# Optimization experiments

Measured on AMD Instinct MI355X. Metric: run time of the kernel, lower is better.

Reference implementation:

```python
import jax, jax.numpy as jnp
import numpy as np

B, L, V, D = 8, 128, 32000, 64
R1, R2, UP = 2 * D, 5 * D, 10 * D  # first_reduce, second_reduce, up_scale defaults


def pos_enc(seq_len, d, n=10000.0):
    # matches getPositionEncoding: P[k,2i]=sin(k/n^(2i/d)), P[k,2i+1]=cos(k/n^(2i/d))
    k = jnp.arange(seq_len, dtype=jnp.float32)[:, None]
    i = jnp.arange(d // 2, dtype=jnp.float32)[None, :]
    ang = k / (n ** (2.0 * i / d))
    return jnp.stack([jnp.sin(ang), jnp.cos(ang)], axis=-1).reshape(seq_len, d)


def setup_inputs() -> dict:
    key = jax.random.key(0)
    ks = jax.random.split(key, 20)

    def lin(k, out_f, in_f):
        bound = 1.0 / np.sqrt(in_f)
        k1, k2 = jax.random.split(k)
        W = jax.random.uniform(k1, (out_f, in_f), jnp.float32, -bound, bound)
        b = jax.random.uniform(k2, (out_f,), jnp.float32, -bound, bound)
        return W, b

    inp = {"x": jax.random.uniform(ks[0], (B, L, V), jnp.float32)}
    inp["W_emb"], inp["b_emb"] = lin(ks[1], D, V)
    inp["W_pos1"], inp["b_pos1"] = lin(ks[2], D, 2 * D)
    inp["W_red"], inp["b_red"] = lin(ks[3], R1, L * D)
    inp["W_pos2"], inp["b_pos2"] = lin(ks[4], R1, 2 * R1)
    inp["W_red2"], inp["b_red2"] = lin(ks[5], R2, L * R1)
    inp["W_pos3"], inp["b_pos3"] = lin(ks[6], R2, 2 * R2)
    inp["W_up1"], inp["b_up1"] = lin(ks[7], UP, R2)
    inp["W_up2"], inp["b_up2"] = lin(ks[8], V, UP)
    inp["W_fin"], inp["b_fin"] = lin(ks[9], 1, L)
    return inp


def reference(x, W_emb, b_emb, W_pos1, b_pos1, W_red, b_red, W_pos2, b_pos2,
              W_red2, b_red2, W_pos3, b_pos3, W_up1, b_up1, W_up2, b_up2,
              W_fin, b_fin):
    relu = jax.nn.relu
    P1 = pos_enc(L, 2 * D)   # [L, 2D]
    P2 = pos_enc(L, 2 * R1)  # [L, 2*R1]
    P3 = pos_enc(L, 2 * R2)  # [L, 2*R2]

    h = relu(x @ W_emb.T + b_emb)                       # [B, L, D]
    h = h + relu(P1 @ W_pos1.T + b_pos1)[None]          # learned sin pos emb

    # einsum('bij,bkm->bikj'): out[b,i,k,j] = h[b,i,j] * sum_m h[b,k,m]
    s = h.sum(-1)                                       # [B, L]
    h = (h[:, :, None, :] * s[:, None, :, None]).reshape(B, L, L * D)
    h = relu(h @ W_red.T + b_red)                       # [B, L, R1]
    h = h + relu(P2 @ W_pos2.T + b_pos2)[None]

    s = h.sum(-1)                                       # [B, L]
    h = (h[:, :, None, :] * s[:, None, :, None]).reshape(B, L, L * R1)
    h = relu(h @ W_red2.T + b_red2)                     # [B, L, R2]
    h = h + relu(P3 @ W_pos3.T + b_pos3)[None]

    h = relu(h @ W_up1.T + b_up1)                       # [B, L, UP]
    h = relu(h @ W_up2.T + b_up2)                       # [B, L, V]
    # transpose(1,2) then Linear(L->1), relu, squeeze
    out = relu(jnp.einsum('blv,l->bv', h, W_fin[0]) + b_fin[0])  # [B, V]
    return out
```

## Files before the change

kernel.cpp:

```cpp
#include <hip/hip_runtime.h>
#include <hip/hip_bf16.h>
#include <math.h>

#define B_  8
#define L_  128
#define V_  32000
#define D_  64
#define R1_ 128
#define R2_ 320
#define UP_ 640
#define SPLITS_ 50

typedef short bf16x8 __attribute__((ext_vector_type(8)));
typedef float f32x4 __attribute__((ext_vector_type(4)));

#define GLDS16(gp, lp)                                                         \
    __builtin_amdgcn_global_load_lds(                                          \
        (const __attribute__((address_space(1))) void*)(gp),                   \
        (__attribute__((address_space(3))) void*)(lp), 16, 0, 0)

static __device__ inline unsigned short f2bf(float x) {
    __hip_bfloat16 h = __float2bfloat16(x);
    return *reinterpret_cast<unsigned short*>(&h);
}

static __device__ inline void split1(float v, unsigned short& h, unsigned short& l) {
    unsigned short hb = f2bf(v);
    float hf = __uint_as_float(((unsigned int)hb) << 16);
    h = hb;
    l = f2bf(v - hf);
}

__global__ __launch_bounds__(256) void prep_weights(const float* __restrict__ Wemb,
                                                    unsigned short* __restrict__ Whb,
                                                    unsigned short* __restrict__ Wlb,
                                                    const float* __restrict__ Wup2,
                                                    unsigned short* __restrict__ Wup2b) {
    int bx = blockIdx.x, t = threadIdx.x;
    if (bx < 1000) {
        int u = bx * 256 + t;
        int kb = u >> 6, row = u & 63;
        const float* s = Wemb + (size_t)row * 32000 + kb * 8;
        unsigned short h8[8], l8[8];
#pragma unroll
        for (int j = 0; j < 8; ++j) split1(s[j], h8[j], l8[j]);
        *(ushort4*)&Whb[(size_t)u * 8]     = *(ushort4*)&h8[0];
        *(ushort4*)&Whb[(size_t)u * 8 + 4] = *(ushort4*)&h8[4];
        *(ushort4*)&Wlb[(size_t)u * 8]     = *(ushort4*)&l8[0];
        *(ushort4*)&Wlb[(size_t)u * 8 + 4] = *(ushort4*)&l8[4];
    } else {
        const int n4 = (V_ * UP_) / 4;
        int stride = 4096 * 256;
        for (int i = (bx - 1000) * 256 + t; i < n4; i += stride) {
            float4 v = ((const float4*)Wup2)[i];
            ushort4 o;
            o.x = f2bf(v.x); o.y = f2bf(v.y); o.z = f2bf(v.z); o.w = f2bf(v.w);
            ((ushort4*)Wup2b)[i] = o;
        }
    }
}

__global__ __launch_bounds__(320) void pe_all(const float* __restrict__ W1,
                                              const float* __restrict__ b1,
                                              float* __restrict__ o1,
                                              const float* __restrict__ W2,
                                              const float* __restrict__ b2,
                                              float* __restrict__ o2,
                                              const float* __restrict__ W3,
                                              const float* __restrict__ b3,
                                              float* __restrict__ o3) {
    __shared__ float P[640];
    int l = blockIdx.x;
    int stage = blockIdx.y;
    const float* W = (stage == 0) ? W1 : (stage == 1) ? W2 : W3;
    const float* bias = (stage == 0) ? b1 : (stage == 1) ? b2 : b3;
    float* out = (stage == 0) ? o1 : (stage == 1) ? o2 : o3;
    int outF = (stage == 0) ? 64 : (stage == 1) ? 128 : 320;
    int dEnc = 2 * outF;
    int t = threadIdx.x;
    for (int m = t; m < dEnc; m += 320) {
        int i = m >> 1;
        float ang = (float)l * powf(10000.0f, -2.0f * (float)i / (float)dEnc);
        P[m] = (m & 1) ? cosf(ang) : sinf(ang);
    }
    __syncthreads();
    if (t < outF) {
        float acc = bias[t];
        const float4* w = (const float4*)(W + (size_t)t * dEnc);
        for (int m4 = 0; m4 < dEnc / 4; ++m4) {
            float4 wv = w[m4];
            float4 pv = *(const float4*)&P[m4 * 4];
            acc = fmaf(pv.x, wv.x, acc);
            acc = fmaf(pv.y, wv.y, acc);
            acc = fmaf(pv.z, wv.z, acc);
            acc = fmaf(pv.w, wv.w, acc);
        }
        out[l * outF + t] = fmaxf(acc, 0.f);
    }
}

__global__ __launch_bounds__(256) void embA_mfma(const float* __restrict__ x,
                                                 const unsigned short* __restrict__ Whb,
                                                 const unsigned short* __restrict__ Wlb,
                                                 float* __restrict__ partA) {
    __shared__ short lds[16384];
    int t = threadIdx.x;
    int lane = t & 63, w = t >> 6;
    int ln = lane & 15, lg = lane >> 4;
    int rb = blockIdx.x, ks = blockIdx.y;
    int row0 = rb * 64;
    const float* xrow = x + (size_t)(row0 + w * 16 + ln) * 32000;

    f32x4 acc[4];
#pragma unroll
    for (int nt = 0; nt < 4; ++nt) acc[nt] = (f32x4){0.f, 0.f, 0.f, 0.f};

    float4 xc[4], xn[4];
    {
        int kb0 = (ks * 640) >> 3;
#pragma unroll
        for (int s = 0; s < 4; ++s) {
            int ubase = s * 256 + w * 64;
            const unsigned short* arr = (s < 2) ? Whb : Wlb;
            int uu = (s < 2) ? ubase : (ubase - 512);
            const char* gp = (const char*)arr + ((size_t)kb0 * 64 + uu + lane) * 16;
            char* lp = (char*)lds + ((s < 2) ? 0 : 8192) + uu * 16;
            GLDS16(gp, lp);
        }
        const float* bp = xrow + ks * 640 + lg * 8;
        xc[0] = ((const float4*)bp)[0];
        xc[1] = ((const float4*)bp)[1];
        xc[2] = ((const float4*)(bp + 32))[0];
        xc[3] = ((const float4*)(bp + 32))[1];
    }

#pragma unroll 2
    for (int ch = 0; ch < 10; ++ch) {
        __syncthreads();
        if (ch < 9) {
            int kb0 = (ks * 640 + (ch + 1) * 64) >> 3;
            int p = (ch + 1) & 1;
#pragma unroll
            for (int s = 0; s < 4; ++s) {
                int ubase = s * 256 + w * 64;
                const unsigned short* arr = (s < 2) ? Whb : Wlb;
                int uu = (s < 2) ? ubase : (ubase - 512);
                const char* gp = (const char*)arr + ((size_t)kb0 * 64 + uu + lane) * 16;
                char* lp = (char*)lds + p * 16384 + ((s < 2) ? 0 : 8192) + uu * 16;
                GLDS16(gp, lp);
            }
            const float* bp = xrow + ks * 640 + (ch + 1) * 64 + lg * 8;
            xn[0] = ((const float4*)bp)[0];
            xn[1] = ((const float4*)bp)[1];
            xn[2] = ((const float4*)(bp + 32))[0];
            xn[3] = ((const float4*)(bp + 32))[1];
        }
        bf16x8 ah[2], al[2];
#pragma unroll
        for (int kstep = 0; kstep < 2; ++kstep) {
            float f[8] = {xc[2 * kstep].x, xc[2 * kstep].y, xc[2 * kstep].z, xc[2 * kstep].w,
                          xc[2 * kstep + 1].x, xc[2 * kstep + 1].y, xc[2 * kstep + 1].z,
                          xc[2 * kstep + 1].w};
            unsigned short h8[8], l8[8];
#pragma unroll
            for (int j = 0; j < 8; ++j) split1(f[j], h8[j], l8[j]);
            ah[kstep] = *(bf16x8*)h8;
            al[kstep] = *(bf16x8*)l8;
        }
        const char* buf = (const char*)lds + (ch & 1) * 16384;
#pragma unroll
        for (int kstep = 0; kstep < 2; ++kstep) {
            int g = kstep * 4 + lg;
#pragma unroll
            for (int nt = 0; nt < 4; ++nt) {
                int nrow = nt * 16 + ln;
                bf16x8 bh = *(const bf16x8*)(buf + (g * 64 + nrow) * 16);
                bf16x8 bl = *(const bf16x8*)(buf + 8192 + (g * 64 + nrow) * 16);
                acc[nt] = __builtin_amdgcn_mfma_f32_16x16x32_bf16(ah[kstep], bh, acc[nt], 0, 0, 0);
                acc[nt] = __builtin_amdgcn_mfma_f32_16x16x32_bf16(ah[kstep], bl, acc[nt], 0, 0, 0);
                acc[nt] = __builtin_amdgcn_mfma_f32_16x16x32_bf16(al[kstep], bh, acc[nt], 0, 0, 0);
            }
        }
#pragma unroll
        for (int i = 0; i < 4; ++i) xc[i] = xn[i];
    }
#pragma unroll
    for (int nt = 0; nt < 4; ++nt)
#pragma unroll
        for (int r = 0; r < 4; ++r)
            partA[((size_t)ks * 1024 + row0 + w * 16 + lg * 4 + r) * 64 + nt * 16 + ln] =
                acc[nt][r];
}

__global__ __launch_bounds__(64) void reduceA_kernel(const float* __restrict__ partA,
                                                     const float* __restrict__ bemb,
                                                     const float* __restrict__ pe1,
                                                     float* __restrict__ h1,
                                                     float* __restrict__ s1) {
    int row = blockIdx.x;
    int d = threadIdx.x;
    int l = row & 127;
    float v = bemb[d];
#pragma unroll 5
    for (int s = 0; s < SPLITS_; ++s) v += partA[((size_t)s * 1024 + row) * 64 + d];
    v = fmaxf(v, 0.f) + pe1[l * 64 + d];
    h1[row * 64 + d] = v;
    float sum = v;
    for (int off = 32; off > 0; off >>= 1) sum += __shfl_down(sum, off);
    if (d == 0) s1[row] = sum;
}

__global__ __launch_bounds__(64) void wr1_kernel(const float* __restrict__ Wred,
                                                 const float* __restrict__ s1,
                                                 float* __restrict__ Wr1) {
    __shared__ float ss[8 * 128];
    int r = blockIdx.x;
    int j = threadIdx.x;
    for (int idx = j; idx < 1024; idx += 64) ss[idx] = s1[idx];
    __syncthreads();
    float acc[8];
#pragma unroll
    for (int b = 0; b < 8; ++b) acc[b] = 0.f;
    const float* w = Wred + (size_t)r * 8192 + j;
    for (int k = 0; k < 128; ++k) {
        float wv = w[k * 64];
#pragma unroll
        for (int b = 0; b < 8; ++b) acc[b] = fmaf(ss[b * 128 + k], wv, acc[b]);
    }
#pragma unroll
    for (int b = 0; b < 8; ++b) Wr1[((size_t)b * 128 + r) * 64 + j] = acc[b];
}

__global__ __launch_bounds__(128) void h2_kernel(const float* __restrict__ h1,
                                                 const float* __restrict__ Wr1,
                                                 const float* __restrict__ bred,
                                                 const float* __restrict__ pe2,
                                                 float* __restrict__ h2,
                                                 float* __restrict__ s2) {
    __shared__ float hrow[64];
    __shared__ float red[2];
    int row = blockIdx.x;
    int b = row >> 7, i = row & 127;
    int r = threadIdx.x;
    if (r < 64) hrow[r] = h1[row * 64 + r];
    __syncthreads();
    float acc = bred[r];
    const float4* w = (const float4*)(Wr1 + ((size_t)b * 128 + r) * 64);
#pragma unroll
    for (int j4 = 0; j4 < 16; ++j4) {
        float4 wv = w[j4];
        float4 hv = *(const float4*)&hrow[j4 * 4];
        acc = fmaf(hv.x, wv.x, acc);
        acc = fmaf(hv.y, wv.y, acc);
        acc = fmaf(hv.z, wv.z, acc);
        acc = fmaf(hv.w, wv.w, acc);
    }
    float val = fmaxf(acc, 0.f) + pe2[i * 128 + r];
    h2[row * 128 + r] = val;
    float sum = val;
    for (int off = 32; off > 0; off >>= 1) sum += __shfl_down(sum, off);
    if ((r & 63) == 0) red[r >> 6] = sum;
    __syncthreads();
    if (r == 0) s2[row] = red[0] + red[1];
}

__global__ __launch_bounds__(128) void wr2_kernel(const float* __restrict__ Wred2,
                                                  const float* __restrict__ s2,
                                                  float* __restrict__ Wr2) {
    __shared__ float ss[8 * 128];
    int r = blockIdx.x;
    int j = threadIdx.x;
    for (int idx = j; idx < 1024; idx += 128) ss[idx] = s2[idx];
    __syncthreads();
    float acc[8];
#pragma unroll
    for (int b = 0; b < 8; ++b) acc[b] = 0.f;
    const float* w = Wred2 + (size_t)r * 16384 + j;
    for (int k = 0; k < 128; ++k) {
        float wv = w[k * 128];
#pragma unroll
        for (int b = 0; b < 8; ++b) acc[b] = fmaf(ss[b * 128 + k], wv, acc[b]);
    }
#pragma unroll
    for (int b = 0; b < 8; ++b) Wr2[((size_t)b * 320 + r) * 128 + j] = acc[b];
}

__global__ __launch_bounds__(320) void h3_kernel(const float* __restrict__ h2,
                                                 const float* __restrict__ Wr2,
                                                 const float* __restrict__ bred2,
                                                 const float* __restrict__ pe3,
                                                 float* __restrict__ h3) {
    __shared__ float hrow[128];
    int row = blockIdx.x;
    int b = row >> 7, i = row & 127;
    int r = threadIdx.x;
    if (r < 128) hrow[r] = h2[row * 128 + r];
    __syncthreads();
    float acc = bred2[r];
    const float4* w = (const float4*)(Wr2 + ((size_t)b * 320 + r) * 128);
#pragma unroll
    for (int j4 = 0; j4 < 32; ++j4) {
        float4 wv = w[j4];
        float4 hv = *(const float4*)&hrow[j4 * 4];
        acc = fmaf(hv.x, wv.x, acc);
        acc = fmaf(hv.y, wv.y, acc);
        acc = fmaf(hv.z, wv.z, acc);
        acc = fmaf(hv.w, wv.w, acc);
    }
    h3[(size_t)row * 320 + r] = fmaxf(acc, 0.f) + pe3[i * 320 + r];
}

__global__ __launch_bounds__(320) void h4_kernel(const float* __restrict__ h3,
                                                 const float* __restrict__ Wup1,
                                                 const float* __restrict__ bup1,
                                                 unsigned short* __restrict__ h4b) {
    __shared__ float hsT[320 * 4];
    int t = threadIdx.x;
    int row0 = blockIdx.x * 4;
    int u = blockIdx.y * 320 + t;
    for (int idx = t; idx < 1280; idx += 320) {
        int q = idx / 320, j = idx - q * 320;
        hsT[j * 4 + q] = h3[(size_t)(row0 + q) * 320 + j];
    }
    __syncthreads();
    float acc[4] = {0.f, 0.f, 0.f, 0.f};
    const float4* w = (const float4*)(Wup1 + (size_t)u * 320);
#pragma unroll 2
    for (int j4 = 0; j4 < 80; ++j4) {
        float4 wv = w[j4];
#pragma unroll
        for (int e = 0; e < 4; ++e) {
            float wc = (e == 0) ? wv.x : (e == 1) ? wv.y : (e == 2) ? wv.z : wv.w;
            float4 hv = *(const float4*)&hsT[(j4 * 4 + e) * 4];
            acc[0] = fmaf(hv.x, wc, acc[0]);
            acc[1] = fmaf(hv.y, wc, acc[1]);
            acc[2] = fmaf(hv.z, wc, acc[2]);
            acc[3] = fmaf(hv.w, wc, acc[3]);
        }
    }
    float bias = bup1[u];
#pragma unroll
    for (int q = 0; q < 4; ++q)
        h4b[(size_t)(row0 + q) * 640 + u] = f2bf(fmaxf(acc[q] + bias, 0.f));
}

__global__ __launch_bounds__(512) void final_mfma_kernel(
    const unsigned short* __restrict__ h4b,
    const unsigned short* __restrict__ Wup2b,
    const float* __restrict__ bup2,
    const float* __restrict__ Wfin,
    const float* __restrict__ bfin,
    float* __restrict__ out) {
    __shared__ short tile[24576];
    __shared__ float redbuf[2][2][128];

    int t = threadIdx.x;
    int lane = t & 63;
    int w = t >> 6;
    int wv = w >> 2;
    int wq = w & 3;
    int bl_ = wq >> 1, lh = wq & 1;
    int ln = lane & 15, lg = lane >> 4;
    int b0 = blockIdx.y * 2;
    int v0 = blockIdx.x * 128;

    f32x4 acc[4][4];
#pragma unroll
    for (int mt = 0; mt < 4; ++mt)
#pragma unroll
        for (int nt = 0; nt < 4; ++nt) acc[mt][nt] = (f32x4){0.f, 0.f, 0.f, 0.f};

    for (int ch = 0; ch < 10; ++ch) {
        int k0 = ch * 64;
        __syncthreads();
#pragma unroll
        for (int s = 0; s < 6; ++s) {
            int F = (w * 6 + s) * 1024 + lane * 16;
            int region = F >> 14;
            int rr = (F >> 7) & 127;
            int g = ((F >> 4) & 7) ^ (rr & 7);
            size_t rowG = (region == 0) ? (size_t)(v0 + rr)
                                        : (size_t)((b0 + region - 1) * 128 + rr);
            const unsigned short* base = (region == 0) ? Wup2b : h4b;
            const char* gp = (const char*)base + (rowG * 640 + (size_t)(k0 + g * 8)) * 2;
            char* lp = (char*)tile + (w * 6 + s) * 1024;
            GLDS16(gp, lp);
        }
        __syncthreads();
#pragma unroll
        for (int ks = 0; ks < 2; ++ks) {
            bf16x8 aF[4], bF[4];
#pragma unroll
            for (int mt = 0; mt < 4; ++mt) {
                int rA = wv * 64 + mt * 16 + ln;
                int g = ks * 4 + lg;
                int off = rA * 128 + ((g ^ (rA & 7)) * 16);
                aF[mt] = *(const bf16x8*)((const char*)tile + off);
            }
#pragma unroll
            for (int nt = 0; nt < 4; ++nt) {
                int rB = lh * 64 + nt * 16 + ln;
                int g = ks * 4 + lg;
                int off = (1 + bl_) * 16384 + rB * 128 + ((g ^ (rB & 7)) * 16);
                bF[nt] = *(const bf16x8*)((const char*)tile + off);
            }
#pragma unroll
            for (int mt = 0; mt < 4; ++mt)
#pragma unroll
                for (int nt = 0; nt < 4; ++nt)
                    acc[mt][nt] = __builtin_amdgcn_mfma_f32_16x16x32_bf16(
                        aF[mt], bF[nt], acc[mt][nt], 0, 0, 0);
        }
    }

    float bfin0 = bfin[0];
#pragma unroll
    for (int mt = 0; mt < 4; ++mt) {
        float bu[4];
#pragma unroll
        for (int r = 0; r < 4; ++r)
            bu[r] = bup2[v0 + wv * 64 + mt * 16 + lg * 4 + r];
        float part[4] = {0.f, 0.f, 0.f, 0.f};
#pragma unroll
        for (int nt = 0; nt < 4; ++nt) {
            float wf = Wfin[lh * 64 + nt * 16 + ln];
#pragma unroll
            for (int r = 0; r < 4; ++r)
                part[r] += wf * fmaxf(acc[mt][nt][r] + bu[r], 0.f);
        }
#pragma unroll
        for (int off = 8; off >= 1; off >>= 1)
#pragma unroll
            for (int r = 0; r < 4; ++r) part[r] += __shfl_xor(part[r], off, 64);
        if (ln == 0) {
#pragma unroll
            for (int r = 0; r < 4; ++r)
                redbuf[bl_][lh][wv * 64 + mt * 16 + lg * 4 + r] = part[r];
        }
    }
    __syncthreads();
    if (t < 256) {
        int bb = t >> 7, v = t & 127;
        float vsum = redbuf[bb][0][v] + redbuf[bb][1][v] + bfin0;
        out[(size_t)(b0 + bb) * 32000 + v0 + v] = fmaxf(vsum, 0.f);
    }
}

extern "C" void kernel_launch(void* const* d_in, const int* in_sizes, int n_in,
                              void* d_out, int out_size, void* d_ws, size_t ws_size,
                              hipStream_t stream) {
    const float* x      = (const float*)d_in[0];
    const float* W_emb  = (const float*)d_in[1];
    const float* b_emb  = (const float*)d_in[2];
    const float* W_pos1 = (const float*)d_in[3];
    const float* b_pos1 = (const float*)d_in[4];
    const float* W_red  = (const float*)d_in[5];
    const float* b_red  = (const float*)d_in[6];
    const float* W_pos2 = (const float*)d_in[7];
    const float* b_pos2 = (const float*)d_in[8];
    const float* W_red2 = (const float*)d_in[9];
    const float* b_red2 = (const float*)d_in[10];
    const float* W_pos3 = (const float*)d_in[11];
    const float* b_pos3 = (const float*)d_in[12];
    const float* W_up1  = (const float*)d_in[13];
    const float* b_up1  = (const float*)d_in[14];
    const float* W_up2  = (const float*)d_in[15];
    const float* b_up2  = (const float*)d_in[16];
    const float* W_fin  = (const float*)d_in[17];
    const float* b_fin  = (const float*)d_in[18];
    float* out = (float*)d_out;

    float* ws  = (float*)d_ws;
    float* pe1 = ws;
    float* pe2 = pe1 + 8192;
    float* pe3 = pe2 + 16384;
    float* h1  = pe3 + 40960;
    float* s1  = h1 + 65536;
    float* Wr1 = s1 + 1024;
    float* h2  = Wr1 + 65536;
    float* s2  = h2 + 131072;
    float* Wr2 = s2 + 1024;
    float* h3  = Wr2 + 327680;
    unsigned short* h4b   = (unsigned short*)(h3 + 327680);
    unsigned short* Wup2b = (unsigned short*)((float*)h4b + 327680);
    float* after = (float*)Wup2b + 10240000;
    unsigned short* Whb = (unsigned short*)after;
    unsigned short* Wlb = Whb + 2048000;
    float* partA = (float*)(Wlb + 2048000);

    prep_weights<<<dim3(5096), 256, 0, stream>>>(W_emb, Whb, Wlb, W_up2, Wup2b);
    pe_all<<<dim3(128, 3), 320, 0, stream>>>(W_pos1, b_pos1, pe1, W_pos2, b_pos2,
                                             pe2, W_pos3, b_pos3, pe3);
    embA_mfma<<<dim3(16, SPLITS_), 256, 0, stream>>>(x, Whb, Wlb, partA);
    reduceA_kernel<<<dim3(1024), 64, 0, stream>>>(partA, b_emb, pe1, h1, s1);
    wr1_kernel<<<dim3(128), 64, 0, stream>>>(W_red, s1, Wr1);
    h2_kernel<<<dim3(1024), 128, 0, stream>>>(h1, Wr1, b_red, pe2, h2, s2);
    wr2_kernel<<<dim3(320), 128, 0, stream>>>(W_red2, s2, Wr2);
    h3_kernel<<<dim3(1024), 320, 0, stream>>>(h2, Wr2, b_red2, pe3, h3);
    h4_kernel<<<dim3(256, 2), 320, 0, stream>>>(h3, W_up1, b_up1, h4b);
    final_mfma_kernel<<<dim3(250, 4), 512, 0, stream>>>(h4b, Wup2b, b_up2, W_fin,
                                                        b_fin, out);
}
```

Measured before the change: 472.9 us.

## Double-buffer final MFMA K-loop, merge prep and pos-enc kernels, add unrolls

The final GEMM's LDS tile is split into two half-size buffers with 32-wide K chunks, so the global-to-LDS load of the next chunk is issued before computing on the current one, and one barrier per iteration is dropped. The weight-prep and positional-encoding kernels are merged into a single launch with 320-thread blocks, removing one kernel launch. Unroll pragmas are added or raised in the reduce and Wr kernels. Smaller K chunks double the iteration count and barriers, and the merged prep kernel makes every block allocate shared memory and use the larger block size.

```diff
diff --git a/kernel.cpp b/kernel.cpp
--- a/kernel.cpp
+++ b/kernel.cpp
@@ -31,14 +31,24 @@
     l = f2bf(v - hf);
 }
 
-__global__ __launch_bounds__(256) void prep_weights(const float* __restrict__ Wemb,
-                                                    unsigned short* __restrict__ Whb,
-                                                    unsigned short* __restrict__ Wlb,
-                                                    const float* __restrict__ Wup2,
-                                                    unsigned short* __restrict__ Wup2b) {
+__global__ __launch_bounds__(320) void prep_all(const float* __restrict__ Wemb,
+                                                unsigned short* __restrict__ Whb,
+                                                unsigned short* __restrict__ Wlb,
+                                                const float* __restrict__ Wup2,
+                                                unsigned short* __restrict__ Wup2b,
+                                                const float* __restrict__ W1,
+                                                const float* __restrict__ b1,
+                                                float* __restrict__ o1,
+                                                const float* __restrict__ W2,
+                                                const float* __restrict__ b2,
+                                                float* __restrict__ o2,
+                                                const float* __restrict__ W3,
+                                                const float* __restrict__ b3,
+                                                float* __restrict__ o3) {
+    __shared__ float P[640];
     int bx = blockIdx.x, t = threadIdx.x;
-    if (bx < 1000) {
-        int u = bx * 256 + t;
+    if (bx < 800) {
+        int u = bx * 320 + t;
         int kb = u >> 6, row = u & 63;
         const float* s = Wemb + (size_t)row * 32000 + kb * 8;
         unsigned short h8[8], l8[8];
@@ -48,54 +58,43 @@
         *(ushort4*)&Whb[(size_t)u * 8 + 4] = *(ushort4*)&h8[4];
         *(ushort4*)&Wlb[(size_t)u * 8]     = *(ushort4*)&l8[0];
         *(ushort4*)&Wlb[(size_t)u * 8 + 4] = *(ushort4*)&l8[4];
+    } else if (bx < 1184) {
+        int id = bx - 800;
+        int l = id & 127;
+        int stage = id >> 7;
+        const float* W = (stage == 0) ? W1 : (stage == 1) ? W2 : W3;
+        const float* bias = (stage == 0) ? b1 : (stage == 1) ? b2 : b3;
+        float* out = (stage == 0) ? o1 : (stage == 1) ? o2 : o3;
+        int outF = (stage == 0) ? 64 : (stage == 1) ? 128 : 320;
+        int dEnc = 2 * outF;
+        for (int m = t; m < dEnc; m += 320) {
+            int i = m >> 1;
+            float ang = (float)l * powf(10000.0f, -2.0f * (float)i / (float)dEnc);
+            P[m] = (m & 1) ? cosf(ang) : sinf(ang);
+        }
+        __syncthreads();
+        if (t < outF) {
+            float acc = bias[t];
+            const float4* w = (const float4*)(W + (size_t)t * dEnc);
+            for (int m4 = 0; m4 < dEnc / 4; ++m4) {
+                float4 wv = w[m4];
+                float4 pv = *(const float4*)&P[m4 * 4];
+                acc = fmaf(pv.x, wv.x, acc);
+                acc = fmaf(pv.y, wv.y, acc);
+                acc = fmaf(pv.z, wv.z, acc);
+                acc = fmaf(pv.w, wv.w, acc);
+            }
+            out[l * outF + t] = fmaxf(acc, 0.f);
+        }
     } else {
         const int n4 = (V_ * UP_) / 4;
-        int stride = 4096 * 256;
-        for (int i = (bx - 1000) * 256 + t; i < n4; i += stride) {
+        int stride = 3200 * 320;
+        for (int i = (bx - 1184) * 320 + t; i < n4; i += stride) {
             float4 v = ((const float4*)Wup2)[i];
             ushort4 o;
             o.x = f2bf(v.x); o.y = f2bf(v.y); o.z = f2bf(v.z); o.w = f2bf(v.w);
             ((ushort4*)Wup2b)[i] = o;
         }
-    }
-}
-
-__global__ __launch_bounds__(320) void pe_all(const float* __restrict__ W1,
-                                              const float* __restrict__ b1,
-                                              float* __restrict__ o1,
-                                              const float* __restrict__ W2,
-                                              const float* __restrict__ b2,
-                                              float* __restrict__ o2,
-                                              const float* __restrict__ W3,
-                                              const float* __restrict__ b3,
-                                              float* __restrict__ o3) {
-    __shared__ float P[640];
-    int l = blockIdx.x;
-    int stage = blockIdx.y;
-    const float* W = (stage == 0) ? W1 : (stage == 1) ? W2 : W3;
-    const float* bias = (stage == 0) ? b1 : (stage == 1) ? b2 : b3;
-    float* out = (stage == 0) ? o1 : (stage == 1) ? o2 : o3;
-    int outF = (stage == 0) ? 64 : (stage == 1) ? 128 : 320;
-    int dEnc = 2 * outF;
-    int t = threadIdx.x;
-    for (int m = t; m < dEnc; m += 320) {
-        int i = m >> 1;
-        float ang = (float)l * powf(10000.0f, -2.0f * (float)i / (float)dEnc);
-        P[m] = (m & 1) ? cosf(ang) : sinf(ang);
-    }
-    __syncthreads();
-    if (t < outF) {
-        float acc = bias[t];
-        const float4* w = (const float4*)(W + (size_t)t * dEnc);
-        for (int m4 = 0; m4 < dEnc / 4; ++m4) {
-            float4 wv = w[m4];
-            float4 pv = *(const float4*)&P[m4 * 4];
-            acc = fmaf(pv.x, wv.x, acc);
-            acc = fmaf(pv.y, wv.y, acc);
-            acc = fmaf(pv.z, wv.z, acc);
-            acc = fmaf(pv.w, wv.w, acc);
-        }
-        out[l * outF + t] = fmaxf(acc, 0.f);
     }
 }
 
@@ -201,7 +200,7 @@
     int d = threadIdx.x;
     int l = row & 127;
     float v = bemb[d];
-#pragma unroll 5
+#pragma unroll 10
     for (int s = 0; s < SPLITS_; ++s) v += partA[((size_t)s * 1024 + row) * 64 + d];
     v = fmaxf(v, 0.f) + pe1[l * 64 + d];
     h1[row * 64 + d] = v;
@@ -222,6 +221,7 @@
 #pragma unroll
     for (int b = 0; b < 8; ++b) acc[b] = 0.f;
     const float* w = Wred + (size_t)r * 8192 + j;
+#pragma unroll 8
     for (int k = 0; k < 128; ++k) {
         float wv = w[k * 64];
 #pragma unroll
@@ -276,6 +276,7 @@
 #pragma unroll
     for (int b = 0; b < 8; ++b) acc[b] = 0.f;
     const float* w = Wred2 + (size_t)r * 16384 + j;
+#pragma unroll 8
     for (int k = 0; k < 128; ++k) {
         float wv = w[k * 128];
 #pragma unroll
@@ -351,7 +352,7 @@
     const float* __restrict__ Wfin,
     const float* __restrict__ bfin,
     float* __restrict__ out) {
-    __shared__ short tile[24576];
+    __shared__ short tile[2][12288];
     __shared__ float redbuf[2][2][128];
 
     int t = threadIdx.x;
@@ -370,47 +371,48 @@
 #pragma unroll
         for (int nt = 0; nt < 4; ++nt) acc[mt][nt] = (f32x4){0.f, 0.f, 0.f, 0.f};
 
-    for (int ch = 0; ch < 10; ++ch) {
-        int k0 = ch * 64;
-        __syncthreads();
-#pragma unroll
-        for (int s = 0; s < 6; ++s) {
-            int F = (w * 6 + s) * 1024 + lane * 16;
-            int region = F >> 14;
-            int rr = (F >> 7) & 127;
-            int g = ((F >> 4) & 7) ^ (rr & 7);
+    auto stage = [&](int ch, int p) {
+#pragma unroll
+        for (int s = 0; s < 3; ++s) {
+            int F = (w * 3 + s) * 1024 + lane * 16;
+            int region = F >> 13;
+            int rr = (F >> 6) & 127;
+            int g = ((F >> 4) & 3) ^ (rr & 3);
             size_t rowG = (region == 0) ? (size_t)(v0 + rr)
                                         : (size_t)((b0 + region - 1) * 128 + rr);
             const unsigned short* base = (region == 0) ? Wup2b : h4b;
-            const char* gp = (const char*)base + (rowG * 640 + (size_t)(k0 + g * 8)) * 2;
-            char* lp = (char*)tile + (w * 6 + s) * 1024;
+            const char* gp =
+                (const char*)base + (rowG * 640 + (size_t)(ch * 32 + g * 8)) * 2;
+            char* lp = (char*)&tile[p][0] + (w * 3 + s) * 1024;
             GLDS16(gp, lp);
         }
+    };
+
+    stage(0, 0);
+
+#pragma unroll 2
+    for (int ch = 0; ch < 20; ++ch) {
         __syncthreads();
-#pragma unroll
-        for (int ks = 0; ks < 2; ++ks) {
-            bf16x8 aF[4], bF[4];
-#pragma unroll
-            for (int mt = 0; mt < 4; ++mt) {
-                int rA = wv * 64 + mt * 16 + ln;
-                int g = ks * 4 + lg;
-                int off = rA * 128 + ((g ^ (rA & 7)) * 16);
-                aF[mt] = *(const bf16x8*)((const char*)tile + off);
-            }
-#pragma unroll
-            for (int nt = 0; nt < 4; ++nt) {
-                int rB = lh * 64 + nt * 16 + ln;
-                int g = ks * 4 + lg;
-                int off = (1 + bl_) * 16384 + rB * 128 + ((g ^ (rB & 7)) * 16);
-                bF[nt] = *(const bf16x8*)((const char*)tile + off);
-            }
-#pragma unroll
-            for (int mt = 0; mt < 4; ++mt)
-#pragma unroll
-                for (int nt = 0; nt < 4; ++nt)
-                    acc[mt][nt] = __builtin_amdgcn_mfma_f32_16x16x32_bf16(
-                        aF[mt], bF[nt], acc[mt][nt], 0, 0, 0);
-        }
+        if (ch < 19) stage(ch + 1, (ch + 1) & 1);
+        const char* buf = (const char*)&tile[ch & 1][0];
+        bf16x8 aF[4], bF[4];
+#pragma unroll
+        for (int mt = 0; mt < 4; ++mt) {
+            int rA = wv * 64 + mt * 16 + ln;
+            aF[mt] = *(const bf16x8*)(buf + rA * 64 + ((lg ^ (rA & 3)) * 16));
+        }
+#pragma unroll
+        for (int nt = 0; nt < 4; ++nt) {
+            int rB = lh * 64 + nt * 16 + ln;
+            bF[nt] = *(const bf16x8*)(buf + 8192 * (1 + bl_) + rB * 64 +
+                                      ((lg ^ (rB & 3)) * 16));
+        }
+#pragma unroll
+        for (int mt = 0; mt < 4; ++mt)
+#pragma unroll
+            for (int nt = 0; nt < 4; ++nt)
+                acc[mt][nt] = __builtin_amdgcn_mfma_f32_16x16x32_bf16(
+                    aF[mt], bF[nt], acc[mt][nt], 0, 0, 0);
     }
 
     float bfin0 = bfin[0];
@@ -488,8 +490,8 @@
     unsigned short* Wlb = Whb + 2048000;
     float* partA = (float*)(Wlb + 2048000);
 
-    prep_weights<<<dim3(5096), 256, 0, stream>>>(W_emb, Whb, Wlb, W_up2, Wup2b);
-    pe_all<<<dim3(128, 3), 320, 0, stream>>>(W_pos1, b_pos1, pe1, W_pos2, b_pos2,
+    prep_all<<<dim3(4384), 320, 0, stream>>>(W_emb, Whb, Wlb, W_up2, Wup2b,
+                                             W_pos1, b_pos1, pe1, W_pos2, b_pos2,
                                              pe2, W_pos3, b_pos3, pe3);
     embA_mfma<<<dim3(16, SPLITS_), 256, 0, stream>>>(x, Whb, Wlb, partA);
     reduceA_kernel<<<dim3(1024), 64, 0, stream>>>(partA, b_emb, pe1, h1, s1);
```

Result: no change. 463.8 us (-1.9%).
